# Kernel optimization log

Hardware: AMD Instinct MI355X
Metric: run time of the kernel (lower is better)

The kernel has to match this reference:

```python
import jax, jax.numpy as jnp
import numpy as np

H = 1024
BATCH, T = 16, 2048

def setup_inputs() -> dict:
    key = jax.random.key(0)
    k1, k2, k3, k4 = jax.random.split(key, 4)
    scale = 1.0 / (H ** 0.5)
    return {
        "u_sequence": jax.random.normal(k1, (BATCH, T, 1), dtype=jnp.float32),
        "A": jax.random.normal(k2, (H, H), dtype=jnp.float32) * scale,
        "B": jax.random.normal(k3, (H, 1), dtype=jnp.float32) * scale,
        "C": jax.random.normal(k4, (1, H), dtype=jnp.float32) * scale,
        "D": jnp.zeros((1,), dtype=jnp.float32),
    }

def reference(u_sequence, A, B, C, D):
    # u_sequence: [Bt, T, 1]
    u = u_sequence[..., 0]            # [Bt, T]
    b_vec = B[:, 0]                   # [H]

    def step(h, u_t):
        # h: [Bt, H], u_t: [Bt]
        h_new = h @ A.T + u_t[:, None] * b_vec[None, :]
        return h_new, h_new

    h0 = jnp.zeros((u.shape[0], H), dtype=u.dtype)
    _, h_stack = jax.lax.scan(step, h0, u.T)   # h_stack: [T, Bt, H]
    h_stack = jnp.swapaxes(h_stack, 0, 1)      # [Bt, T, H]
    y = jnp.einsum("bth,h->bt", h_stack, C[0]) + u * D[0]
    return y[..., None]                         # [Bt, T, 1]
```

## Files before the change

### kernel.cpp

```cpp
#include <hip/hip_runtime.h>

#define HDIM 1024
#define TLEN 2048
#define NBATCH 16

typedef short bf16x8 __attribute__((ext_vector_type(8)));
typedef float floatx4 __attribute__((ext_vector_type(4)));
typedef unsigned short ushort_t;

__device__ __forceinline__ ushort_t f2bf(float x) {
  unsigned u = __float_as_uint(x);
  unsigned r = (u + 0x7FFFu + ((u >> 16) & 1u)) >> 16;
  return (ushort_t)r;
}
__device__ __forceinline__ float bf2f(ushort_t h) {
  return __uint_as_float(((unsigned)h) << 16);
}

typedef __attribute__((address_space(1))) void gvoid_t;
typedef __attribute__((address_space(3))) void lvoid_t;
__device__ __forceinline__ void gload16(const ushort_t* g, ushort_t* l) {
  __builtin_amdgcn_global_load_lds((gvoid_t*)g, (lvoid_t*)l, 16, 0, 0);
}

#define TSTR 71

__global__ __launch_bounds__(256) void prep(const float* __restrict__ A,
    const float* __restrict__ Bv, const float* __restrict__ Cv,
    ushort_t* __restrict__ Ah, ushort_t* __restrict__ Am, ushort_t* __restrict__ Al,
    ushort_t* __restrict__ ATh, ushort_t* __restrict__ ATm, ushort_t* __restrict__ ATl,
    float* __restrict__ Vc, float* __restrict__ U) {
  __shared__ ushort_t Lt[3 * 64 * TSTR];
  const int tid = threadIdx.x;
  if (blockIdx.x >= 256) {
    int i = (blockIdx.x - 256) * 256 + tid;
    if (i < HDIM) Vc[i] = Bv[i];
    else U[i - HDIM] = Cv[i - HDIM];
    return;
  }
  const int row0 = (blockIdx.x >> 4) * 64, col0 = (blockIdx.x & 15) * 64;
  const int r = tid >> 2, q = tid & 3;
  ushort_t hs[16], ms[16], ls[16];
#pragma unroll
  for (int c4 = 0; c4 < 4; ++c4) {
    float4 a = *(const float4*)&A[(row0 + r) * HDIM + col0 + q * 16 + c4 * 4];
    float av[4] = {a.x, a.y, a.z, a.w};
#pragma unroll
    for (int i = 0; i < 4; ++i) {
      float z = av[i];
      ushort_t h = f2bf(z); float r1 = z - bf2f(h);
      ushort_t mq = f2bf(r1); float r2 = r1 - bf2f(mq);
      ushort_t lq = f2bf(r2);
      hs[c4 * 4 + i] = h; ms[c4 * 4 + i] = mq; ls[c4 * 4 + i] = lq;
    }
  }
  size_t go = (size_t)(row0 + r) * HDIM + col0 + q * 16;
  *(uint4*)&Ah[go] = ((uint4*)hs)[0]; *(uint4*)&Ah[go + 8] = ((uint4*)hs)[1];
  *(uint4*)&Am[go] = ((uint4*)ms)[0]; *(uint4*)&Am[go + 8] = ((uint4*)ms)[1];
  *(uint4*)&Al[go] = ((uint4*)ls)[0]; *(uint4*)&Al[go + 8] = ((uint4*)ls)[1];
#pragma unroll
  for (int i = 0; i < 16; ++i) {
    int c = q * 16 + i;
    Lt[0 * 64 * TSTR + r * TSTR + c] = hs[i];
    Lt[1 * 64 * TSTR + r * TSTR + c] = ms[i];
    Lt[2 * 64 * TSTR + r * TSTR + c] = ls[i];
  }
  __syncthreads();
  const int c = tid >> 2, q2 = tid & 3;
  ushort_t* dsts[3] = {ATh, ATm, ATl};
#pragma unroll
  for (int s = 0; s < 3; ++s) {
    ushort_t tmp[16];
#pragma unroll
    for (int rr = 0; rr < 16; ++rr) tmp[rr] = Lt[s * 64 * TSTR + (q2 * 16 + rr) * TSTR + c];
    size_t gt = (size_t)(col0 + c) * HDIM + row0 + q2 * 16;
    *(uint4*)&dsts[s][gt] = ((uint4*)tmp)[0];
    *(uint4*)&dsts[s][gt + 8] = ((uint4*)tmp)[1];
  }
}

template <int MODE, int NC, bool SIX, bool WRITEL, bool WROW>
__global__ __launch_bounds__(256) void sq_mfma(
    const ushort_t* __restrict__ Xh, const ushort_t* __restrict__ Xm,
    const ushort_t* __restrict__ Xl,
    const ushort_t* __restrict__ XTh, const ushort_t* __restrict__ XTm,
    const ushort_t* __restrict__ XTl,
    ushort_t* __restrict__ Zh, ushort_t* __restrict__ Zm, ushort_t* __restrict__ Zl,
    ushort_t* __restrict__ ZTh, ushort_t* __restrict__ ZTm, ushort_t* __restrict__ ZTl,
    const float* __restrict__ Af, const float* __restrict__ Bvf,
    float* __restrict__ VU) {
  constexpr int BK = SIX ? 32 : 64;
  constexpr int SLAB = 64 * BK;
  constexpr int BUFSTR = (SIX ? 6 : 4) * SLAB;
  constexpr int BBASE = (SIX ? 3 : 2) * SLAB;
  constexpr int LDS_ELEMS = 2 * BUFSTR;
  __shared__ __align__(16) ushort_t sm[LDS_ELEMS];
  const int tid = threadIdx.x;

  if (blockIdx.x >= 256) {
    const int tb = blockIdx.x - 256;
    const int wv = tb * 4 + (tid >> 6);
    const int lane = tid & 63;
    if (MODE == 0) {
      float acc = 0.f;
      for (int k = lane; k < HDIM; k += 64) acc += Af[(size_t)wv * HDIM + k] * Bvf[k];
      for (int off = 32; off; off >>= 1) acc += __shfl_down(acc, off);
      if (lane == 0) VU[HDIM + wv] = acc;
    } else {
      const ushort_t* Ph = (MODE == 1) ? Xh : XTh;
      const ushort_t* Pm = (MODE == 1) ? Xm : XTm;
      float acc[NC];
#pragma unroll
      for (int n = 0; n < NC; ++n) acc[n] = 0.f;
      for (int k = lane; k < HDIM; k += 64) {
        float a = bf2f(Ph[(size_t)wv * HDIM + k]) + bf2f(Pm[(size_t)wv * HDIM + k]);
#pragma unroll
        for (int n = 0; n < NC; ++n) acc[n] += a * VU[(size_t)n * HDIM + k];
      }
#pragma unroll
      for (int n = 0; n < NC; ++n) {
        float s = acc[n];
        for (int off = 32; off; off >>= 1) s += __shfl_down(s, off);
        if (lane == 0) VU[(size_t)(NC + n) * HDIM + wv] = s;
      }
    }
    return;
  }

  const int bb = blockIdx.x;
  const int xcd = bb & 7, slot = bb >> 3;
  const int tr = 4 * (xcd >> 1) + (slot >> 3);
  const int tc = 8 * (xcd & 1) + (slot & 7);
  const int row0 = tr * 64, col0 = tc * 64;

  const int w = tid >> 6, l = tid & 63, li = l & 15, quad = l >> 4;

  floatx4 acc0 = {0.f, 0.f, 0.f, 0.f}, acc1 = acc0, acc2 = acc0, acc3 = acc0;

  ushort_t* lwb = &sm[w * 512];

  if (SIX) {
    const int sr = tid >> 2, sq4 = tid & 3;
    const int aoff = (w * 16 + li) * 32 + quad * 8;
    const int b0o = (0 * 16 + li) * 32 + quad * 8;
    const int b1o = (1 * 16 + li) * 32 + quad * 8;
    const int b2o = (2 * 16 + li) * 32 + quad * 8;
    const int b3o = (3 * 16 + li) * 32 + quad * 8;

    const ushort_t* gAh = Xh + (size_t)(row0 + sr) * HDIM + sq4 * 8;
    const ushort_t* gAm = Xm + (size_t)(row0 + sr) * HDIM + sq4 * 8;
    const ushort_t* gAl = Xl + (size_t)(row0 + sr) * HDIM + sq4 * 8;
    const ushort_t* gBh = XTh + (size_t)(col0 + sr) * HDIM + sq4 * 8;
    const ushort_t* gBm = XTm + (size_t)(col0 + sr) * HDIM + sq4 * 8;
    const ushort_t* gBl = XTl + (size_t)(col0 + sr) * HDIM + sq4 * 8;

    {
      ushort_t* lb = lwb;
      gload16(gAh, lb);
      gload16(gAm, lb + SLAB);
      gload16(gAl, lb + 2 * SLAB);
      gload16(gBh, lb + BBASE);
      gload16(gBm, lb + BBASE + SLAB);
      gload16(gBl, lb + BBASE + 2 * SLAB);
    }
    __syncthreads();

    int cur = 0;
    for (int k0 = 0; k0 < HDIM; k0 += 32) {
      if (k0 + 32 < HDIM) {
        ushort_t* lb = lwb + (cur ^ 1) * BUFSTR;
        const int kn = k0 + 32;
        gload16(gAh + kn, lb);
        gload16(gAm + kn, lb + SLAB);
        gload16(gAl + kn, lb + 2 * SLAB);
        gload16(gBh + kn, lb + BBASE);
        gload16(gBm + kn, lb + BBASE + SLAB);
        gload16(gBl + kn, lb + BBASE + 2 * SLAB);
      }
      const int cb = cur * BUFSTR;
      bf16x8 ah = *(const bf16x8*)&sm[cb + aoff];
      bf16x8 am = *(const bf16x8*)&sm[cb + SLAB + aoff];
      bf16x8 al = *(const bf16x8*)&sm[cb + 2 * SLAB + aoff];
      {
        bf16x8 bh = *(const bf16x8*)&sm[cb + BBASE + b0o];
        bf16x8 bm = *(const bf16x8*)&sm[cb + BBASE + SLAB + b0o];
        bf16x8 bl = *(const bf16x8*)&sm[cb + BBASE + 2 * SLAB + b0o];
        acc0 = __builtin_amdgcn_mfma_f32_16x16x32_bf16(ah, bh, acc0, 0, 0, 0);
        acc0 = __builtin_amdgcn_mfma_f32_16x16x32_bf16(ah, bm, acc0, 0, 0, 0);
        acc0 = __builtin_amdgcn_mfma_f32_16x16x32_bf16(am, bh, acc0, 0, 0, 0);
        acc0 = __builtin_amdgcn_mfma_f32_16x16x32_bf16(am, bm, acc0, 0, 0, 0);
        acc0 = __builtin_amdgcn_mfma_f32_16x16x32_bf16(ah, bl, acc0, 0, 0, 0);
        acc0 = __builtin_amdgcn_mfma_f32_16x16x32_bf16(al, bh, acc0, 0, 0, 0);
      }
      {
        bf16x8 bh = *(const bf16x8*)&sm[cb + BBASE + b1o];
        bf16x8 bm = *(const bf16x8*)&sm[cb + BBASE + SLAB + b1o];
        bf16x8 bl = *(const bf16x8*)&sm[cb + BBASE + 2 * SLAB + b1o];
        acc1 = __builtin_amdgcn_mfma_f32_16x16x32_bf16(ah, bh, acc1, 0, 0, 0);
        acc1 = __builtin_amdgcn_mfma_f32_16x16x32_bf16(ah, bm, acc1, 0, 0, 0);
        acc1 = __builtin_amdgcn_mfma_f32_16x16x32_bf16(am, bh, acc1, 0, 0, 0);
        acc1 = __builtin_amdgcn_mfma_f32_16x16x32_bf16(am, bm, acc1, 0, 0, 0);
        acc1 = __builtin_amdgcn_mfma_f32_16x16x32_bf16(ah, bl, acc1, 0, 0, 0);
        acc1 = __builtin_amdgcn_mfma_f32_16x16x32_bf16(al, bh, acc1, 0, 0, 0);
      }
      {
        bf16x8 bh = *(const bf16x8*)&sm[cb + BBASE + b2o];
        bf16x8 bm = *(const bf16x8*)&sm[cb + BBASE + SLAB + b2o];
        bf16x8 bl = *(const bf16x8*)&sm[cb + BBASE + 2 * SLAB + b2o];
        acc2 = __builtin_amdgcn_mfma_f32_16x16x32_bf16(ah, bh, acc2, 0, 0, 0);
        acc2 = __builtin_amdgcn_mfma_f32_16x16x32_bf16(ah, bm, acc2, 0, 0, 0);
        acc2 = __builtin_amdgcn_mfma_f32_16x16x32_bf16(am, bh, acc2, 0, 0, 0);
        acc2 = __builtin_amdgcn_mfma_f32_16x16x32_bf16(am, bm, acc2, 0, 0, 0);
        acc2 = __builtin_amdgcn_mfma_f32_16x16x32_bf16(ah, bl, acc2, 0, 0, 0);
        acc2 = __builtin_amdgcn_mfma_f32_16x16x32_bf16(al, bh, acc2, 0, 0, 0);
      }
      {
        bf16x8 bh = *(const bf16x8*)&sm[cb + BBASE + b3o];
        bf16x8 bm = *(const bf16x8*)&sm[cb + BBASE + SLAB + b3o];
        bf16x8 bl = *(const bf16x8*)&sm[cb + BBASE + 2 * SLAB + b3o];
        acc3 = __builtin_amdgcn_mfma_f32_16x16x32_bf16(ah, bh, acc3, 0, 0, 0);
        acc3 = __builtin_amdgcn_mfma_f32_16x16x32_bf16(ah, bm, acc3, 0, 0, 0);
        acc3 = __builtin_amdgcn_mfma_f32_16x16x32_bf16(am, bh, acc3, 0, 0, 0);
        acc3 = __builtin_amdgcn_mfma_f32_16x16x32_bf16(am, bm, acc3, 0, 0, 0);
        acc3 = __builtin_amdgcn_mfma_f32_16x16x32_bf16(ah, bl, acc3, 0, 0, 0);
        acc3 = __builtin_amdgcn_mfma_f32_16x16x32_bf16(al, bh, acc3, 0, 0, 0);
      }
      __syncthreads();
      cur ^= 1;
    }
  } else {
    const int sr8 = tid >> 3;
    const int kq8 = (tid & 7) ^ (sr8 & 7);
    const ushort_t* gAh = Xh + (size_t)(row0 + sr8) * HDIM + kq8 * 8;
    const ushort_t* gAm = Xm + (size_t)(row0 + sr8) * HDIM + kq8 * 8;
    const ushort_t* gBh = XTh + (size_t)(col0 + sr8) * HDIM + kq8 * 8;
    const ushort_t* gBm = XTm + (size_t)(col0 + sr8) * HDIM + kq8 * 8;
    const size_t p1 = (size_t)32 * HDIM;

    const int j0 = (quad ^ (li & 7)) * 8;
    const int aoff = (w * 16 + li) * 64 + j0;
    const int b0o = (0 * 16 + li) * 64 + j0;
    const int b1o = (1 * 16 + li) * 64 + j0;
    const int b2o = (2 * 16 + li) * 64 + j0;
    const int b3o = (3 * 16 + li) * 64 + j0;

    {
      ushort_t* lb = lwb;
      gload16(gAh, lb);              gload16(gAh + p1, lb + 2048);
      gload16(gAm, lb + SLAB);       gload16(gAm + p1, lb + SLAB + 2048);
      gload16(gBh, lb + BBASE);      gload16(gBh + p1, lb + BBASE + 2048);
      gload16(gBm, lb + BBASE + SLAB); gload16(gBm + p1, lb + BBASE + SLAB + 2048);
    }
    __syncthreads();

    int cur = 0;
    for (int k0 = 0; k0 < HDIM; k0 += 64) {
      if (k0 + 64 < HDIM) {
        ushort_t* lb = lwb + (cur ^ 1) * BUFSTR;
        const int kn = k0 + 64;
        gload16(gAh + kn, lb);              gload16(gAh + p1 + kn, lb + 2048);
        gload16(gAm + kn, lb + SLAB);       gload16(gAm + p1 + kn, lb + SLAB + 2048);
        gload16(gBh + kn, lb + BBASE);      gload16(gBh + p1 + kn, lb + BBASE + 2048);
        gload16(gBm + kn, lb + BBASE + SLAB); gload16(gBm + p1 + kn, lb + BBASE + SLAB + 2048);
      }
      const int cb = cur * BUFSTR;
#pragma unroll
      for (int cc = 0; cc < 2; ++cc) {
        const int cx = cc * 32;
        bf16x8 ah = *(const bf16x8*)&sm[cb + (aoff ^ cx)];
        bf16x8 am = *(const bf16x8*)&sm[cb + SLAB + (aoff ^ cx)];
        {
          bf16x8 bh = *(const bf16x8*)&sm[cb + BBASE + (b0o ^ cx)];
          bf16x8 bm = *(const bf16x8*)&sm[cb + BBASE + SLAB + (b0o ^ cx)];
          acc0 = __builtin_amdgcn_mfma_f32_16x16x32_bf16(ah, bh, acc0, 0, 0, 0);
          acc0 = __builtin_amdgcn_mfma_f32_16x16x32_bf16(ah, bm, acc0, 0, 0, 0);
          acc0 = __builtin_amdgcn_mfma_f32_16x16x32_bf16(am, bh, acc0, 0, 0, 0);
          acc0 = __builtin_amdgcn_mfma_f32_16x16x32_bf16(am, bm, acc0, 0, 0, 0);
        }
        {
          bf16x8 bh = *(const bf16x8*)&sm[cb + BBASE + (b1o ^ cx)];
          bf16x8 bm = *(const bf16x8*)&sm[cb + BBASE + SLAB + (b1o ^ cx)];
          acc1 = __builtin_amdgcn_mfma_f32_16x16x32_bf16(ah, bh, acc1, 0, 0, 0);
          acc1 = __builtin_amdgcn_mfma_f32_16x16x32_bf16(ah, bm, acc1, 0, 0, 0);
          acc1 = __builtin_amdgcn_mfma_f32_16x16x32_bf16(am, bh, acc1, 0, 0, 0);
          acc1 = __builtin_amdgcn_mfma_f32_16x16x32_bf16(am, bm, acc1, 0, 0, 0);
        }
        {
          bf16x8 bh = *(const bf16x8*)&sm[cb + BBASE + (b2o ^ cx)];
          bf16x8 bm = *(const bf16x8*)&sm[cb + BBASE + SLAB + (b2o ^ cx)];
          acc2 = __builtin_amdgcn_mfma_f32_16x16x32_bf16(ah, bh, acc2, 0, 0, 0);
          acc2 = __builtin_amdgcn_mfma_f32_16x16x32_bf16(ah, bm, acc2, 0, 0, 0);
          acc2 = __builtin_amdgcn_mfma_f32_16x16x32_bf16(am, bh, acc2, 0, 0, 0);
          acc2 = __builtin_amdgcn_mfma_f32_16x16x32_bf16(am, bm, acc2, 0, 0, 0);
        }
        {
          bf16x8 bh = *(const bf16x8*)&sm[cb + BBASE + (b3o ^ cx)];
          bf16x8 bm = *(const bf16x8*)&sm[cb + BBASE + SLAB + (b3o ^ cx)];
          acc3 = __builtin_amdgcn_mfma_f32_16x16x32_bf16(ah, bh, acc3, 0, 0, 0);
          acc3 = __builtin_amdgcn_mfma_f32_16x16x32_bf16(ah, bm, acc3, 0, 0, 0);
          acc3 = __builtin_amdgcn_mfma_f32_16x16x32_bf16(am, bh, acc3, 0, 0, 0);
          acc3 = __builtin_amdgcn_mfma_f32_16x16x32_bf16(am, bm, acc3, 0, 0, 0);
        }
      }
      __syncthreads();
      cur ^= 1;
    }
  }

  floatx4 accs[4] = {acc0, acc1, acc2, acc3};
#pragma unroll
  for (int j = 0; j < 4; ++j) {
#pragma unroll
    for (int e = 0; e < 4; ++e) {
      float z = accs[j][e];
      int rl = w * 16 + quad * 4 + e;
      int cl = j * 16 + li;
      size_t go = (size_t)(row0 + rl) * HDIM + col0 + cl;
      ushort_t h = f2bf(z); float r1 = z - bf2f(h);
      ushort_t mq = f2bf(r1);
      if (WROW) { Zh[go] = h; Zm[go] = mq; }
      sm[0 * 64 * TSTR + rl * TSTR + cl] = h;
      sm[1 * 64 * TSTR + rl * TSTR + cl] = mq;
      if (WRITEL) {
        ushort_t lq = f2bf(r1 - bf2f(mq));
        if (WROW) Zl[go] = lq;
        sm[2 * 64 * TSTR + rl * TSTR + cl] = lq;
      }
    }
  }
  __syncthreads();
  const int c = tid >> 2, q2 = tid & 3;
  ushort_t* dsts[3] = {ZTh, ZTm, ZTl};
  const int npass = WRITEL ? 3 : 2;
#pragma unroll
  for (int s = 0; s < 3; ++s) {
    if (s >= npass) break;
    ushort_t tmp[16];
#pragma unroll
    for (int rr = 0; rr < 16; ++rr) tmp[rr] = sm[s * 64 * TSTR + (q2 * 16 + rr) * TSTR + c];
    size_t gt = (size_t)(col0 + c) * HDIM + row0 + q2 * 16;
    *(uint4*)&dsts[s][gt] = ((uint4*)tmp)[0];
    *(uint4*)&dsts[s][gt + 8] = ((uint4*)tmp)[1];
  }
}

__global__ __launch_bounds__(256) void utail8(const ushort_t* __restrict__ PTh,
                                              const ushort_t* __restrict__ PTm,
                                              float* __restrict__ U, int dstbase) {
  const int wv = blockIdx.x * 4 + (threadIdx.x >> 6);
  const int lane = threadIdx.x & 63;
  float acc[8];
#pragma unroll
  for (int m = 0; m < 8; ++m) acc[m] = 0.f;
  const float* Usrc = U + (size_t)(dstbase - 8) * HDIM;
  for (int k = lane; k < HDIM; k += 64) {
    float a = bf2f(PTh[(size_t)wv * HDIM + k]) + bf2f(PTm[(size_t)wv * HDIM + k]);
#pragma unroll
    for (int m = 0; m < 8; ++m) acc[m] += a * Usrc[(size_t)m * HDIM + k];
  }
#pragma unroll
  for (int m = 0; m < 8; ++m) {
    float s = acc[m];
    for (int off = 32; off; off >>= 1) s += __shfl_down(s, off);
    if (lane == 0) U[(size_t)(dstbase + m) * HDIM + wv] = s;
  }
}

__global__ __launch_bounds__(256) void wavedotK(const float* __restrict__ U,
                                                const float* __restrict__ Vc,
                                                float* __restrict__ Km) {
  int wv = (blockIdx.x * blockDim.x + threadIdx.x) >> 6;
  int lane = threadIdx.x & 63;
  if (wv >= 32 * 64) return;
  int mr = wv >> 6;
  int nc = wv & 63;
  float s = 0.f;
  for (int k = lane; k < HDIM; k += 64) s += U[mr * HDIM + k] * Vc[nc * HDIM + k];
  for (int off = 32; off; off >>= 1) s += __shfl_down(s, off);
  if (lane == 0) Km[wv] = s;
}

__global__ __launch_bounds__(256) void convk2(const float* __restrict__ u,
                                              const float* __restrict__ Km,
                                              const float* __restrict__ Dv,
                                              float* __restrict__ y) {
  __shared__ float ks[256];
  __shared__ float us[512];
  const int tt = threadIdx.x;
  const int t0 = blockIdx.x * 256;
  const int b = blockIdx.y;
  const float* ub = u + (size_t)b * TLEN;
  const int t = t0 + tt;
  float s0 = Dv[0] * ub[t], s1 = 0.f, s2 = 0.f, s3 = 0.f;
  for (int mc = 0; mc <= t0; mc += 256) {
    __syncthreads();
    ks[tt] = Km[mc + tt];
    int w0 = t0 - mc - 255;
    int g0 = w0 + tt;
    us[tt] = (g0 >= 0) ? ub[g0] : 0.f;
    int g1 = w0 + 256 + tt;
    us[256 + tt] = (g1 < TLEN) ? ub[g1] : 0.f;
    __syncthreads();
    if (mc < t0) {
#pragma unroll 4
      for (int r = 0; r < 256; r += 4) {
        float4 kv = *(const float4*)&ks[r];
        s0 += kv.x * us[tt - r + 255];
        s1 += kv.y * us[tt - r + 254];
        s2 += kv.z * us[tt - r + 253];
        s3 += kv.w * us[tt - r + 252];
      }
    } else {
      for (int r = 0; r <= tt; ++r) s0 += ks[r] * us[tt - r + 255];
    }
  }
  y[(size_t)b * TLEN + t] = s0 + s1 + s2 + s3;
}

extern "C" void kernel_launch(void* const* d_in, const int* in_sizes, int n_in,
                              void* d_out, int out_size, void* d_ws, size_t ws_size,
                              hipStream_t stream) {
  const float* u  = (const float*)d_in[0];
  const float* A  = (const float*)d_in[1];
  const float* Bv = (const float*)d_in[2];
  const float* Cv = (const float*)d_in[3];
  const float* Dv = (const float*)d_in[4];
  float* out = (float*)d_out;

  char* wsb = (char*)d_ws;
  size_t off = 0;
  ushort_t* S[2][6];
  for (int s = 0; s < 2; ++s)
    for (int a = 0; a < 6; ++a) { S[s][a] = (ushort_t*)(wsb + off); off += (size_t)2 << 20; }
  float* Vc = (float*)(wsb + off); off += 64 * HDIM * 4;
  float* U  = (float*)(wsb + off); off += 32 * HDIM * 4;
  float* Km = (float*)(wsb + off); off += TLEN * 4;

  const dim3 gsq(512);

#define SQ(MODE, NC, SIX, WRL, WROW, IN, OUT, VU)                              \
  sq_mfma<MODE, NC, SIX, WRL, WROW><<<gsq, 256, 0, stream>>>(                  \
      S[IN][0], S[IN][1], S[IN][2], S[IN][3], S[IN][4], S[IN][5],              \
      S[OUT][0], S[OUT][1], S[OUT][2], S[OUT][3], S[OUT][4], S[OUT][5],        \
      A, Bv, VU)

  prep<<<dim3(264), 256, 0, stream>>>(A, Bv, Cv,
      S[0][0], S[0][1], S[0][2], S[0][3], S[0][4], S[0][5], Vc, U);

  SQ(0, 1,  true,  true,  true,  0, 1, Vc);
  SQ(1, 2,  true,  true,  true,  1, 0, Vc);
  SQ(1, 4,  true,  true,  true,  0, 1, Vc);
  SQ(1, 8,  true,  false, true,  1, 0, Vc);
  SQ(1, 16, false, false, true,  0, 1, Vc);
  SQ(1, 32, false, false, true,  1, 0, Vc);
  SQ(2, 1,  false, false, true,  0, 1, U);
  SQ(2, 2,  false, false, true,  1, 0, U);
  SQ(2, 4,  false, false, false, 0, 1, U);
#undef SQ

  utail8<<<dim3(256), 256, 0, stream>>>(S[1][3], S[1][4], U, 8);
  utail8<<<dim3(256), 256, 0, stream>>>(S[1][3], S[1][4], U, 16);
  utail8<<<dim3(256), 256, 0, stream>>>(S[1][3], S[1][4], U, 24);

  wavedotK<<<dim3(512), 256, 0, stream>>>(U, Vc, Km);
  convk2<<<dim3(TLEN / 256, NBATCH), 256, 0, stream>>>(u, Km, Dv, out);
}
```

Baseline: 351.6 us.

## Extend squaring chain one step and merge utail launches into one 16-column tail

Adds another repeated-squaring stage with NC=8 in the U chain, so the final U columns come from a single 16-wide tail kernel instead of three sequential 8-wide launches. It also stages the shared VU vector chunks in LDS for the MODE 1 side-block matvec, so the four waves in a block read them once. The intent is to cut serial launches and redundant global reads. The cost is one more full squaring kernel, which writes the power needed by the tail, plus extra __syncthreads in the side blocks.

```diff
diff --git a/kernel.cpp b/kernel.cpp
--- a/kernel.cpp
+++ b/kernel.cpp
@@ -106,9 +106,32 @@
       for (int k = lane; k < HDIM; k += 64) acc += Af[(size_t)wv * HDIM + k] * Bvf[k];
       for (int off = 32; off; off >>= 1) acc += __shfl_down(acc, off);
       if (lane == 0) VU[HDIM + wv] = acc;
+    } else if (MODE == 1) {
+      float* Vs = (float*)sm;
+      const ushort_t* Ph = Xh;
+      const ushort_t* Pm = Xm;
+      float acc[NC];
+#pragma unroll
+      for (int n = 0; n < NC; ++n) acc[n] = 0.f;
+      for (int k0 = 0; k0 < HDIM; k0 += 64) {
+        __syncthreads();
+        for (int idx = tid; idx < NC * 64; idx += 256)
+          Vs[idx] = VU[(size_t)(idx >> 6) * HDIM + k0 + (idx & 63)];
+        __syncthreads();
+        const int k = k0 + lane;
+        float a = bf2f(Ph[(size_t)wv * HDIM + k]) + bf2f(Pm[(size_t)wv * HDIM + k]);
+#pragma unroll
+        for (int n = 0; n < NC; ++n) acc[n] += a * Vs[n * 64 + lane];
+      }
+#pragma unroll
+      for (int n = 0; n < NC; ++n) {
+        float s = acc[n];
+        for (int off = 32; off; off >>= 1) s += __shfl_down(s, off);
+        if (lane == 0) VU[(size_t)(NC + n) * HDIM + wv] = s;
+      }
     } else {
-      const ushort_t* Ph = (MODE == 1) ? Xh : XTh;
-      const ushort_t* Pm = (MODE == 1) ? Xm : XTm;
+      const ushort_t* Ph = XTh;
+      const ushort_t* Pm = XTm;
       float acc[NC];
 #pragma unroll
       for (int n = 0; n < NC; ++n) acc[n] = 0.f;
@@ -344,25 +367,24 @@
   }
 }
 
-__global__ __launch_bounds__(256) void utail8(const ushort_t* __restrict__ PTh,
-                                              const ushort_t* __restrict__ PTm,
-                                              float* __restrict__ U, int dstbase) {
+__global__ __launch_bounds__(256) void utail16(const ushort_t* __restrict__ PTh,
+                                               const ushort_t* __restrict__ PTm,
+                                               float* __restrict__ U) {
   const int wv = blockIdx.x * 4 + (threadIdx.x >> 6);
   const int lane = threadIdx.x & 63;
-  float acc[8];
-#pragma unroll
-  for (int m = 0; m < 8; ++m) acc[m] = 0.f;
-  const float* Usrc = U + (size_t)(dstbase - 8) * HDIM;
+  float acc[16];
+#pragma unroll
+  for (int m = 0; m < 16; ++m) acc[m] = 0.f;
   for (int k = lane; k < HDIM; k += 64) {
     float a = bf2f(PTh[(size_t)wv * HDIM + k]) + bf2f(PTm[(size_t)wv * HDIM + k]);
 #pragma unroll
-    for (int m = 0; m < 8; ++m) acc[m] += a * Usrc[(size_t)m * HDIM + k];
-  }
-#pragma unroll
-  for (int m = 0; m < 8; ++m) {
+    for (int m = 0; m < 16; ++m) acc[m] += a * U[(size_t)m * HDIM + k];
+  }
+#pragma unroll
+  for (int m = 0; m < 16; ++m) {
     float s = acc[m];
     for (int off = 32; off; off >>= 1) s += __shfl_down(s, off);
-    if (lane == 0) U[(size_t)(dstbase + m) * HDIM + wv] = s;
+    if (lane == 0) U[(size_t)(16 + m) * HDIM + wv] = s;
   }
 }
 
@@ -455,12 +477,11 @@
   SQ(1, 32, false, false, true,  1, 0, Vc);
   SQ(2, 1,  false, false, true,  0, 1, U);
   SQ(2, 2,  false, false, true,  1, 0, U);
-  SQ(2, 4,  false, false, false, 0, 1, U);
+  SQ(2, 4,  false, false, true,  0, 1, U);
+  SQ(2, 8,  false, false, false, 1, 0, U);
 #undef SQ
 
-  utail8<<<dim3(256), 256, 0, stream>>>(S[1][3], S[1][4], U, 8);
-  utail8<<<dim3(256), 256, 0, stream>>>(S[1][3], S[1][4], U, 16);
-  utail8<<<dim3(256), 256, 0, stream>>>(S[1][3], S[1][4], U, 24);
+  utail16<<<dim3(256), 256, 0, stream>>>(S[0][3], S[0][4], U);
 
   wavedotK<<<dim3(512), 256, 0, stream>>>(U, Vc, Km);
   convk2<<<dim3(TLEN / 256, NBATCH), 256, 0, stream>>>(u, Km, Dv, out);
```

Result: faster. 329.0 us (-6.4%).
